# Kernel tuning notes

Measured on AMD Instinct MI355X. Metric: run time of the kernel, lower is better.

Reference implementation:

```python
import jax, jax.numpy as jnp
import numpy as np


def setup_inputs() -> dict:
    key = jax.random.key(0)
    ks = jax.random.split(key, 8)
    B, L, D, H = 4, 2048, 4096, 8
    BW = D // H
    std = 1.0 / np.sqrt(BW)
    x = jax.random.normal(ks[0], (B, L, D), dtype=jnp.float32)
    segment_pos = jax.random.randint(ks[1], (B, L), 0, 1024)
    prev_h = jax.random.normal(ks[2], (B, D), dtype=jnp.float32)
    w_in = jax.random.normal(ks[3], (H, BW, BW), dtype=jnp.float32) * std
    b_in = jnp.zeros((H, BW), dtype=jnp.float32)
    w_a = jax.random.normal(ks[4], (H, BW, BW), dtype=jnp.float32) * std
    b_a = jnp.zeros((H, BW), dtype=jnp.float32)
    # a_param init: uniform on ring [0.9, 0.999], softplus-inverse transform
    unif = jax.random.uniform(ks[5], (D,), dtype=jnp.float32)
    min_rad, max_rad = 0.9, 0.999
    a_real = 0.5 * jnp.log(unif * (max_rad**2 - min_rad**2) + min_rad**2 + 1e-8)
    a_param = jnp.log(jnp.exp(-a_real) - 1.0)
    return {"x": x, "segment_pos": segment_pos, "prev_h": prev_h,
            "w_in": w_in, "b_in": b_in, "w_a": w_a, "b_a": b_a,
            "a_param": a_param}


def _block_diag_linear(x, w, b):
    # x: [B,L,D]; w: [H,BW,BW]; b: [H,BW]
    B, L, D = x.shape
    H = w.shape[0]
    xr = x.reshape(B, L, H, D // H)
    y = jnp.einsum('blhi,hij->blhj', xr, w) + b
    return y.reshape(B, L, D)


def reference(x, segment_pos, prev_h, w_in, b_in, w_a, b_a, a_param):
    # reset indicator at document boundaries (segment_pos == 0)
    reset = (segment_pos == 0).astype(x.dtype)          # [B,L]
    gate_x = jax.nn.sigmoid(_block_diag_linear(x, w_in, b_in))
    gate_a = jax.nn.sigmoid(_block_diag_linear(x, w_a, b_a))
    log_a = -8.0 * gate_a * jax.nn.softplus(a_param)    # [B,L,D]
    a = jnp.exp(log_a)
    multiplier = jnp.sqrt(1.0 - jnp.exp(2.0 * log_a) + 1e-6)
    multiplier = reset[..., None] + (1.0 - reset)[..., None] * multiplier
    normalized_x = x * gate_x * multiplier
    # zero the decay at reset positions (hidden state reset)
    a = a * (1.0 - reset)[..., None]
    # linear recurrence y_t = a_t * y_{t-1} + x_t (initial hidden state = 0,
    # matching the torch L>1 path which does not use prev_h)
    def combine(c1, c2):
        a1, b1 = c1
        a2, b2 = c2
        return (a2 * a1, a2 * b1 + b2)
    _, y = jax.lax.associative_scan(combine, (a, normalized_x), axis=1)
    return y
```

## Files before the change

### kernel.cpp

```cpp
#include <hip/hip_runtime.h>
#include <hip/hip_bf16.h>

typedef _Float16 f16;
typedef _Float16 f16x2 __attribute__((ext_vector_type(2)));
typedef _Float16 f16x4 __attribute__((ext_vector_type(4)));
typedef _Float16 f16x8 __attribute__((ext_vector_type(8)));
typedef float f32x4 __attribute__((ext_vector_type(4)));

#define B_  4
#define L_  2048
#define D_  4096
#define H_  8
#define BW_ 512
#define M_  (B_*L_)
#define CHUNK 128
#define NCH (L_/CHUNK)
#define LOG2E 1.4426950408889634f

static const size_t OFF_WPK   = 0;
static const size_t OFF_MSP   = 8ull<<20;
static const size_t OFF_XH    = 9ull<<20;
static const size_t OFF_YLAP  = 73ull<<20;
static const size_t OFF_SUMA  = 208ull<<20;
static const size_t OFF_SUMY  = 209ull<<20;
static const size_t OFF_CARRY = 210ull<<20;

__device__ __forceinline__ void gl16(const void* g, void* l) {
    __builtin_amdgcn_global_load_lds(
        (const __attribute__((address_space(1))) unsigned int*)g,
        (__attribute__((address_space(3))) unsigned int*)l, 16, 0, 0);
}

__global__ __launch_bounds__(256)
void prep_wpack(const float* __restrict__ w_in, const float* __restrict__ w_a,
                const float* __restrict__ a_param,
                f16* __restrict__ wpk, float* __restrict__ msp2) {
    const int kt  = blockIdx.x & 7;
    const int n32 = (blockIdx.x >> 3) & 15;
    const int h   = blockIdx.x >> 7;
    const int tid = threadIdx.x;
    if (blockIdx.x < 16) {
        int d = blockIdx.x * 256 + tid;
        float v = a_param[d];
        msp2[d] = -8.f * log1pf(expf(v)) * LOG2E;
    }
#pragma unroll
    for (int q = 0; q < 2; ++q) {
        int slot = q * 256 + tid;
        int lane = slot & 63;
        int fidx = slot >> 6;
        int g    = fidx >> 2;
        int fn   = (fidx >> 1) & 1;
        int kk2  = fidx & 1;
        int row = n32 * 32 + fn * 16 + (lane & 15);
        int col = kt * 64 + kk2 * 32 + ((lane >> 4) << 3);
        const float* src = (g ? w_a : w_in) + (size_t)h * BW_ * BW_;
        f16x8 v;
#pragma unroll
        for (int e = 0; e < 8; ++e)
            v[e] = (f16)src[(size_t)(col + e) * BW_ + row];
        size_t o = ((((size_t)(h * 16 + n32) * 8 + kt) * 8) + fidx) * 64 + lane;
        *(f16x8*)(wpk + o * 8) = v;
    }
}

__global__ __launch_bounds__(256)
void prep_xh(const float* __restrict__ x, f16* __restrict__ xh) {
    size_t i = ((size_t)blockIdx.x * 256 + threadIdx.x) * 8;
    size_t stride = (size_t)gridDim.x * 256 * 8;
    for (; i < (size_t)M_ * D_; i += stride) {
        f32x4 v0 = *(const f32x4*)(x + i);
        f32x4 v1 = *(const f32x4*)(x + i + 4);
        f16x8 hv;
        hv[0] = (f16)v0.x; hv[1] = (f16)v0.y; hv[2] = (f16)v0.z; hv[3] = (f16)v0.w;
        hv[4] = (f16)v1.x; hv[5] = (f16)v1.y; hv[6] = (f16)v1.z; hv[7] = (f16)v1.w;
        *(f16x8*)(xh + i) = hv;
    }
}

#define BM 128
#define BN 64
#define BKK 64
#define NT (BW_/BKK)
#define BUFB 16384

#define SMEM_BYTES 36608

__global__ __launch_bounds__(256, 3)
void gemm_gates(const f16*   __restrict__ xh,
                const int*   __restrict__ segpos,
                const f16*   __restrict__ wpk,
                const float* __restrict__ b_in,
                const float* __restrict__ b_a,
                const float* __restrict__ msp2,
                f16x2* __restrict__ ylap,
                float* __restrict__ sumA,
                float* __restrict__ sumY) {
    __shared__ __align__(16) char smem[SMEM_BYTES];
    f16*   om_s = (f16*)smem;
    f16*   xn_s = (f16*)(smem + 16896);
    float* segA = (float*)(smem + 33792);
    float* segY = (float*)(smem + 34944);
    float* rst_s= (float*)(smem + 36096);

    const int tid  = threadIdx.x;
    const int m0   = blockIdx.x * BM;
    const int n0   = blockIdx.y * BN;
    const int h    = blockIdx.z;
    const int lane = tid & 63;
    const int wid  = tid >> 6;
    const int wr   = wid >> 1;
    const int wc   = wid & 1;

    f32x4 accX[4][2] = {};
    f32x4 accA[4][2] = {};

    if (tid < BM) rst_s[tid] = (segpos[m0 + tid] == 0) ? 1.f : 0.f;

    const int grow  = lane >> 3;
    const int gcolS = (((lane & 7) ^ grow) << 3);
    const f16* aSrc = xh + (size_t)(m0 + wid * 32 + grow) * D_ + h * BW_ + gcolS;

    const f16* wbase = wpk + ((size_t)(h * 16) + (n0 >> 5) + wc) * 32768;

    const int swz  = (lane & 7) << 3;
    const int kx   = (lane >> 4) << 3;
    const int arow = wr * 64 + (lane & 15);

    const int rowb = wr * 64 + ((lane >> 4) << 2);
    const int txo = (n0 >> 6) + 1;

    f16x8 bfr[2][8];

    {
        const int k0 = (txo & (NT - 1)) * BKK;
        f16* Asb = (f16*)smem;
#pragma unroll
        for (int q = 0; q < 4; ++q)
            gl16(aSrc + k0 + (size_t)q * 8 * D_, &Asb[(wid * 32 + q * 8) * 64]);
        const f16* tp = wbase + (size_t)(txo & (NT - 1)) * 4096;
#pragma unroll
        for (int j = 0; j < 8; ++j)
            bfr[0][j] = *(const f16x8*)(tp + j * 512 + lane * 8);
    }

#pragma unroll
    for (int t = 0; t < NT; ++t) {
        const int cur = t & 1;
        if (t + 1 < NT) {
            const int kt1 = (t + 1 + txo) & (NT - 1);
            f16* Asb = (f16*)(smem + (cur ^ 1) * BUFB);
#pragma unroll
            for (int q = 0; q < 4; ++q)
                gl16(aSrc + kt1 * BKK + (size_t)q * 8 * D_, &Asb[(wid * 32 + q * 8) * 64]);
            const f16* tp = wbase + (size_t)kt1 * 4096;
#pragma unroll
            for (int j = 0; j < 8; ++j)
                bfr[cur ^ 1][j] = *(const f16x8*)(tp + j * 512 + lane * 8);
            asm volatile("s_waitcnt vmcnt(12)" ::: "memory");
        } else {
            asm volatile("s_waitcnt vmcnt(0)" ::: "memory");
        }
        __builtin_amdgcn_s_barrier();
        __builtin_amdgcn_sched_barrier(0);

        const f16* Asb = (const f16*)(smem + cur * BUFB);
#pragma unroll
        for (int kk2 = 0; kk2 < 2; ++kk2) {
            const int kcolS = (kk2 * 32 + kx) ^ swz;
            f16x8 af[4];
#pragma unroll
            for (int fm = 0; fm < 4; ++fm)
                af[fm] = *(const f16x8*)&Asb[(arow + fm * 16) * 64 + kcolS];
#pragma unroll
            for (int fn = 0; fn < 2; ++fn) {
                f16x8 bx = bfr[cur][fn * 2 + kk2];
                f16x8 ba = bfr[cur][4 + fn * 2 + kk2];
#pragma unroll
                for (int fm = 0; fm < 4; ++fm) {
                    accX[fm][fn] = __builtin_amdgcn_mfma_f32_16x16x32_f16(af[fm], bx, accX[fm][fn], 0, 0, 0);
                    accA[fm][fn] = __builtin_amdgcn_mfma_f32_16x16x32_f16(af[fm], ba, accA[fm][fn], 0, 0, 0);
                }
            }
        }
        __builtin_amdgcn_sched_barrier(0);
        __builtin_amdgcn_s_barrier();
    }

    const f16* As1 = (const f16*)(smem + BUFB);
    f16 xvv[2][4][4];
#pragma unroll
    for (int fn = 0; fn < 2; ++fn) {
        const int ctile = wc * 32 + fn * 16 + (lane & 15);
#pragma unroll
        for (int fm = 0; fm < 4; ++fm)
#pragma unroll
            for (int reg = 0; reg < 4; ++reg) {
                const int rowt = rowb + fm * 16 + reg;
                xvv[fn][fm][reg] = As1[rowt * 64 + (ctile ^ ((rowt & 7) << 3))];
            }
    }
    __syncthreads();

    {
#pragma unroll
        for (int fn = 0; fn < 2; ++fn) {
            const int ctile = wc * 32 + fn * 16 + (lane & 15);
            const int d = h * BW_ + n0 + ctile;
            const float bx = b_in[d];
            const float ba = b_a[d];
            const float mspd = msp2[d];
#pragma unroll
            for (int fm = 0; fm < 4; ++fm) {
#pragma unroll
                for (int reg = 0; reg < 4; ++reg) {
                    const int rowt = rowb + fm * 16 + reg;
                    float gxl = accX[fm][fn][reg] + bx;
                    float gal = accA[fm][fn][reg] + ba;
                    float gx = __builtin_amdgcn_rcpf(1.f + __builtin_amdgcn_exp2f(-gxl * LOG2E));
                    float ga = __builtin_amdgcn_rcpf(1.f + __builtin_amdgcn_exp2f(-gal * LOG2E));
                    float a  = __builtin_amdgcn_exp2f(mspd * ga);
                    float a2 = a * a;
                    float mult = __builtin_amdgcn_sqrtf(1.f + 1e-6f - a2);
                    float rv = rst_s[rowt];
                    a *= (1.f - rv);
                    mult = rv + (1.f - rv) * mult;
                    float xv = (float)xvv[fn][fm][reg];
                    om_s[rowt * 66 + ctile] = (f16)(1.f - a);
                    xn_s[rowt * 66 + ctile] = (f16)(xv * gx * mult);
                }
            }
        }
    }
    __syncthreads();

    const int scol = tid & 63;
    const int sseg = tid >> 6;
    {
        float A = 1.f, yv = 0.f;
#pragma unroll 4
        for (int t = sseg * 32; t < sseg * 32 + 32; ++t) {
            float a  = 1.f - (float)om_s[t * 66 + scol];
            float xn = (float)xn_s[t * 66 + scol];
            yv = fmaf(a, yv, xn);
            A *= a;
        }
        segA[sseg * 72 + scol] = A;
        segY[sseg * 72 + scol] = yv;
    }
    __syncthreads();

    {
        float cy = 0.f, pA = 1.f;
        for (int s = 0; s < sseg; ++s) {
            float As_ = segA[s * 72 + scol];
            float Ys_ = segY[s * 72 + scol];
            cy = fmaf(As_, cy, Ys_);
            pA *= As_;
        }
        float Arun = 1.f, yv = cy;
        const size_t obase = (size_t)(m0 + sseg * 32) * D_ + h * BW_ + n0 + scol;
#pragma unroll 4
        for (int i = 0; i < 32; ++i) {
            const int t = sseg * 32 + i;
            float a  = 1.f - (float)om_s[t * 66 + scol];
            float xn = (float)xn_s[t * 66 + scol];
            yv = fmaf(a, yv, xn);
            Arun *= a;
            f16x2 p;
            p[0] = (f16)yv;
            p[1] = (f16)(pA * Arun);
            ylap[obase + (size_t)i * D_] = p;
        }
        if (sseg == 3) {
            const int bb = m0 >> 11;
            const int cc = (m0 & 2047) >> 7;
            size_t si = ((size_t)bb * NCH + cc) * D_ + h * BW_ + n0 + scol;
            sumA[si] = pA * Arun;
            sumY[si] = yv;
        }
    }
}

__global__ __launch_bounds__(256)
void scan_mid(const float* __restrict__ sumA, const float* __restrict__ sumY,
              float* __restrict__ carry) {
    int d = blockIdx.x * 256 + threadIdx.x;
    int b = blockIdx.y;
    float hcur = 0.f;
#pragma unroll
    for (int c = 0; c < NCH; ++c) {
        size_t si = ((size_t)b * NCH + c) * D_ + d;
        carry[si] = hcur;
        hcur = fmaf(sumA[si], hcur, sumY[si]);
    }
}

__global__ __launch_bounds__(256)
void scan_apply(const float* __restrict__ carry, const f16x2* __restrict__ ylap,
                float* __restrict__ y) {
    size_t i4 = (size_t)blockIdx.x * 256 + threadIdx.x;
    const size_t stride = (size_t)gridDim.x * 256;
    const size_t n4 = (size_t)M_ * D_ / 4;
    for (; i4 < n4; i4 += stride) {
        size_t i = i4 * 4;
        size_t row = i >> 12;
        int d = (int)(i & 4095);
        int b = (int)(row >> 11);
        int c = ((int)row & 2047) >> 7;
        const float* cp = carry + (((size_t)(b * NCH + c)) << 12) + d;
        f32x4 cv = *(const f32x4*)cp;
        f16x8 pk = *(const f16x8*)(ylap + i);
        f32x4 o;
        o.x = fmaf(cv.x, (float)pk[1], (float)pk[0]);
        o.y = fmaf(cv.y, (float)pk[3], (float)pk[2]);
        o.z = fmaf(cv.z, (float)pk[5], (float)pk[4]);
        o.w = fmaf(cv.w, (float)pk[7], (float)pk[6]);
        *(f32x4*)(y + i) = o;
    }
}

extern "C" void kernel_launch(void* const* d_in, const int* in_sizes, int n_in,
                              void* d_out, int out_size, void* d_ws, size_t ws_size,
                              hipStream_t stream) {
    const float* x       = (const float*)d_in[0];
    const int*   segpos  = (const int*)d_in[1];
    const float* w_in    = (const float*)d_in[3];
    const float* b_in    = (const float*)d_in[4];
    const float* w_a     = (const float*)d_in[5];
    const float* b_a     = (const float*)d_in[6];
    const float* a_param = (const float*)d_in[7];

    float* y  = (float*)d_out;
    char*  ws = (char*)d_ws;
    f16*   wpk   = (f16*)(ws + OFF_WPK);
    float* msp2  = (float*)(ws + OFF_MSP);
    f16*   xh    = (f16*)(ws + OFF_XH);
    f16x2* ylap  = (f16x2*)(ws + OFF_YLAP);
    float* sumA  = (float*)(ws + OFF_SUMA);
    float* sumY  = (float*)(ws + OFF_SUMY);
    float* carry = (float*)(ws + OFF_CARRY);

    prep_wpack<<<dim3(1024), 256, 0, stream>>>(w_in, w_a, a_param, wpk, msp2);
    prep_xh<<<dim3(2048), 256, 0, stream>>>(x, xh);
    gemm_gates<<<dim3(M_ / BM, BW_ / BN, H_), 256, 0, stream>>>(
        xh, segpos, wpk, b_in, b_a, msp2, ylap, sumA, sumY);
    scan_mid<<<dim3(D_ / 256, B_), 256, 0, stream>>>(sumA, sumY, carry);
    scan_apply<<<dim3(4096), 256, 0, stream>>>(carry, ylap, y);
}
```

Before: 219.2 us.

## Fuse fp32-to-fp16 conversion of x into GEMM with triple-buffered K pipeline

Drops the separate prep_xh pass that wrote an fp16 copy of x. The gate GEMM now streams fp32 x straight into LDS through global_load_lds, with K tiles cut from 64 to 32 and triple buffering. Values are packed to fp16 in registers before the MFMAs. The grid is reordered so the N-tiles that share an M-tile are adjacent, which should help L2 reuse of x. This removes a full read and write pass over x, at the cost of twice the LDS bytes per K element, more GEMM-side conversion work and round-toward-zero conversion.

```diff
diff --git a/kernel.cpp b/kernel.cpp
--- a/kernel.cpp
+++ b/kernel.cpp
@@ -5,6 +5,7 @@
 typedef _Float16 f16x2 __attribute__((ext_vector_type(2)));
 typedef _Float16 f16x4 __attribute__((ext_vector_type(4)));
 typedef _Float16 f16x8 __attribute__((ext_vector_type(8)));
+typedef __fp16  h16x2 __attribute__((ext_vector_type(2)));
 typedef float f32x4 __attribute__((ext_vector_type(4)));
 
 #define B_  4
@@ -19,11 +20,10 @@
 
 static const size_t OFF_WPK   = 0;
 static const size_t OFF_MSP   = 8ull<<20;
-static const size_t OFF_XH    = 9ull<<20;
-static const size_t OFF_YLAP  = 73ull<<20;
-static const size_t OFF_SUMA  = 208ull<<20;
-static const size_t OFF_SUMY  = 209ull<<20;
-static const size_t OFF_CARRY = 210ull<<20;
+static const size_t OFF_YLAP  = 9ull<<20;
+static const size_t OFF_SUMA  = 144ull<<20;
+static const size_t OFF_SUMY  = 145ull<<20;
+static const size_t OFF_CARRY = 146ull<<20;
 
 __device__ __forceinline__ void gl16(const void* g, void* l) {
     __builtin_amdgcn_global_load_lds(
@@ -64,30 +64,16 @@
     }
 }
 
-__global__ __launch_bounds__(256)
-void prep_xh(const float* __restrict__ x, f16* __restrict__ xh) {
-    size_t i = ((size_t)blockIdx.x * 256 + threadIdx.x) * 8;
-    size_t stride = (size_t)gridDim.x * 256 * 8;
-    for (; i < (size_t)M_ * D_; i += stride) {
-        f32x4 v0 = *(const f32x4*)(x + i);
-        f32x4 v1 = *(const f32x4*)(x + i + 4);
-        f16x8 hv;
-        hv[0] = (f16)v0.x; hv[1] = (f16)v0.y; hv[2] = (f16)v0.z; hv[3] = (f16)v0.w;
-        hv[4] = (f16)v1.x; hv[5] = (f16)v1.y; hv[6] = (f16)v1.z; hv[7] = (f16)v1.w;
-        *(f16x8*)(xh + i) = hv;
-    }
-}
-
 #define BM 128
 #define BN 64
-#define BKK 64
-#define NT (BW_/BKK)
+#define BKK 32
+#define NT 16
 #define BUFB 16384
 
-#define SMEM_BYTES 36608
+#define SMEM_BYTES 49664
 
 __global__ __launch_bounds__(256, 3)
-void gemm_gates(const f16*   __restrict__ xh,
+void gemm_gates(const float* __restrict__ x,
                 const int*   __restrict__ segpos,
                 const f16*   __restrict__ wpk,
                 const float* __restrict__ b_in,
@@ -101,11 +87,11 @@
     f16*   xn_s = (f16*)(smem + 16896);
     float* segA = (float*)(smem + 33792);
     float* segY = (float*)(smem + 34944);
-    float* rst_s= (float*)(smem + 36096);
+    float* rst_s= (float*)(smem + 49152);
 
     const int tid  = threadIdx.x;
-    const int m0   = blockIdx.x * BM;
-    const int n0   = blockIdx.y * BN;
+    const int n0   = blockIdx.x * BN;
+    const int m0   = blockIdx.y * BM;
     const int h    = blockIdx.z;
     const int lane = tid & 63;
     const int wid  = tid >> 6;
@@ -118,86 +104,91 @@
     if (tid < BM) rst_s[tid] = (segpos[m0 + tid] == 0) ? 1.f : 0.f;
 
     const int grow  = lane >> 3;
-    const int gcolS = (((lane & 7) ^ grow) << 3);
-    const f16* aSrc = xh + (size_t)(m0 + wid * 32 + grow) * D_ + h * BW_ + gcolS;
+    const int gcolS = (((lane & 7) ^ grow) << 2);
+    const float* aSrc = x + (size_t)(m0 + wid * 32 + grow) * D_ + h * BW_ + gcolS;
 
     const f16* wbase = wpk + ((size_t)(h * 16) + (n0 >> 5) + wc) * 32768;
 
-    const int swz  = (lane & 7) << 3;
-    const int kx   = (lane >> 4) << 3;
+    const int koff = ((lane >> 4) * 32) ^ ((lane & 7) << 4);
     const int arow = wr * 64 + (lane & 15);
-
     const int rowb = wr * 64 + ((lane >> 4) << 2);
-    const int txo = (n0 >> 6) + 1;
-
-    f16x8 bfr[2][8];
-
-    {
-        const int k0 = (txo & (NT - 1)) * BKK;
-        f16* Asb = (f16*)smem;
-#pragma unroll
-        for (int q = 0; q < 4; ++q)
-            gl16(aSrc + k0 + (size_t)q * 8 * D_, &Asb[(wid * 32 + q * 8) * 64]);
-        const f16* tp = wbase + (size_t)(txo & (NT - 1)) * 4096;
-#pragma unroll
-        for (int j = 0; j < 8; ++j)
-            bfr[0][j] = *(const f16x8*)(tp + j * 512 + lane * 8);
-    }
+    const int txo  = ((n0 >> 5) + 2) & (NT - 1);
+
+    f16x8 bfr[3][4];
+
+#define STAGE(T)                                                              \
+    {                                                                         \
+        const int ktg = ((T) + txo) & (NT - 1);                               \
+        float* Asb = (float*)(smem + ((T) % 3) * BUFB);                       \
+        _Pragma("unroll")                                                     \
+        for (int q = 0; q < 4; ++q)                                           \
+            gl16(aSrc + ktg * 32 + (size_t)q * 8 * D_,                        \
+                 Asb + (wid * 32 + q * 8) * 32);                              \
+        _Pragma("unroll")                                                     \
+        for (int g = 0; g < 2; ++g)                                           \
+            _Pragma("unroll")                                                 \
+            for (int fn = 0; fn < 2; ++fn)                                    \
+                bfr[(T) % 3][g * 2 + fn] = *(const f16x8*)(wbase +            \
+                    ((size_t)(ktg >> 1) * 8 + g * 4 + fn * 2 + (ktg & 1)) *   \
+                        512 + lane * 8);                                      \
+    }
+
+    STAGE(0);
+    STAGE(1);
 
 #pragma unroll
     for (int t = 0; t < NT; ++t) {
-        const int cur = t & 1;
-        if (t + 1 < NT) {
-            const int kt1 = (t + 1 + txo) & (NT - 1);
-            f16* Asb = (f16*)(smem + (cur ^ 1) * BUFB);
-#pragma unroll
-            for (int q = 0; q < 4; ++q)
-                gl16(aSrc + kt1 * BKK + (size_t)q * 8 * D_, &Asb[(wid * 32 + q * 8) * 64]);
-            const f16* tp = wbase + (size_t)kt1 * 4096;
-#pragma unroll
-            for (int j = 0; j < 8; ++j)
-                bfr[cur ^ 1][j] = *(const f16x8*)(tp + j * 512 + lane * 8);
-            asm volatile("s_waitcnt vmcnt(12)" ::: "memory");
-        } else {
-            asm volatile("s_waitcnt vmcnt(0)" ::: "memory");
-        }
+        if (t + 2 < NT) STAGE(t + 2);
+        if (t < NT - 2)      asm volatile("s_waitcnt vmcnt(16)" ::: "memory");
+        else if (t == NT - 2) asm volatile("s_waitcnt vmcnt(8)" ::: "memory");
+        else                  asm volatile("s_waitcnt vmcnt(0)" ::: "memory");
         __builtin_amdgcn_s_barrier();
         __builtin_amdgcn_sched_barrier(0);
 
-        const f16* Asb = (const f16*)(smem + cur * BUFB);
-#pragma unroll
-        for (int kk2 = 0; kk2 < 2; ++kk2) {
-            const int kcolS = (kk2 * 32 + kx) ^ swz;
-            f16x8 af[4];
-#pragma unroll
-            for (int fm = 0; fm < 4; ++fm)
-                af[fm] = *(const f16x8*)&Asb[(arow + fm * 16) * 64 + kcolS];
-#pragma unroll
-            for (int fn = 0; fn < 2; ++fn) {
-                f16x8 bx = bfr[cur][fn * 2 + kk2];
-                f16x8 ba = bfr[cur][4 + fn * 2 + kk2];
-#pragma unroll
-                for (int fm = 0; fm < 4; ++fm) {
-                    accX[fm][fn] = __builtin_amdgcn_mfma_f32_16x16x32_f16(af[fm], bx, accX[fm][fn], 0, 0, 0);
-                    accA[fm][fn] = __builtin_amdgcn_mfma_f32_16x16x32_f16(af[fm], ba, accA[fm][fn], 0, 0, 0);
-                }
+        const char* Asb = smem + (t % 3) * BUFB;
+        f16x8 af[4];
+#pragma unroll
+        for (int fm = 0; fm < 4; ++fm) {
+            const char* rp = Asb + (arow + fm * 16) * 128;
+            f32x4 u0 = *(const f32x4*)(rp + koff);
+            f32x4 u1 = *(const f32x4*)(rp + (koff ^ 16));
+            h16x2 p0 = __builtin_amdgcn_cvt_pkrtz(u0.x, u0.y);
+            h16x2 p1 = __builtin_amdgcn_cvt_pkrtz(u0.z, u0.w);
+            h16x2 p2 = __builtin_amdgcn_cvt_pkrtz(u1.x, u1.y);
+            h16x2 p3 = __builtin_amdgcn_cvt_pkrtz(u1.z, u1.w);
+            f16x8 a8;
+            a8[0] = (f16)p0[0]; a8[1] = (f16)p0[1];
+            a8[2] = (f16)p1[0]; a8[3] = (f16)p1[1];
+            a8[4] = (f16)p2[0]; a8[5] = (f16)p2[1];
+            a8[6] = (f16)p3[0]; a8[7] = (f16)p3[1];
+            af[fm] = a8;
+        }
+#pragma unroll
+        for (int fn = 0; fn < 2; ++fn) {
+            f16x8 bx = bfr[t % 3][fn];
+            f16x8 ba = bfr[t % 3][2 + fn];
+#pragma unroll
+            for (int fm = 0; fm < 4; ++fm) {
+                accX[fm][fn] = __builtin_amdgcn_mfma_f32_16x16x32_f16(af[fm], bx, accX[fm][fn], 0, 0, 0);
+                accA[fm][fn] = __builtin_amdgcn_mfma_f32_16x16x32_f16(af[fm], ba, accA[fm][fn], 0, 0, 0);
             }
         }
         __builtin_amdgcn_sched_barrier(0);
         __builtin_amdgcn_s_barrier();
     }
-
-    const f16* As1 = (const f16*)(smem + BUFB);
-    f16 xvv[2][4][4];
+#undef STAGE
+
+    const float* AsL = (const float*)(smem + (wc ? 0 : 2 * BUFB));
+    float xvv[2][4][4];
 #pragma unroll
     for (int fn = 0; fn < 2; ++fn) {
-        const int ctile = wc * 32 + fn * 16 + (lane & 15);
+        const int c5 = fn * 16 + (lane & 15);
 #pragma unroll
         for (int fm = 0; fm < 4; ++fm)
 #pragma unroll
             for (int reg = 0; reg < 4; ++reg) {
                 const int rowt = rowb + fm * 16 + reg;
-                xvv[fn][fm][reg] = As1[rowt * 64 + (ctile ^ ((rowt & 7) << 3))];
+                xvv[fn][fm][reg] = AsL[rowt * 32 + (c5 ^ ((rowt & 7) << 2))];
             }
     }
     __syncthreads();
@@ -225,7 +216,7 @@
                     float rv = rst_s[rowt];
                     a *= (1.f - rv);
                     mult = rv + (1.f - rv) * mult;
-                    float xv = (float)xvv[fn][fm][reg];
+                    float xv = xvv[fn][fm][reg];
                     om_s[rowt * 66 + ctile] = (f16)(1.f - a);
                     xn_s[rowt * 66 + ctile] = (f16)(xv * gx * mult);
                 }
@@ -335,16 +326,14 @@
     char*  ws = (char*)d_ws;
     f16*   wpk   = (f16*)(ws + OFF_WPK);
     float* msp2  = (float*)(ws + OFF_MSP);
-    f16*   xh    = (f16*)(ws + OFF_XH);
     f16x2* ylap  = (f16x2*)(ws + OFF_YLAP);
     float* sumA  = (float*)(ws + OFF_SUMA);
     float* sumY  = (float*)(ws + OFF_SUMY);
     float* carry = (float*)(ws + OFF_CARRY);
 
     prep_wpack<<<dim3(1024), 256, 0, stream>>>(w_in, w_a, a_param, wpk, msp2);
-    prep_xh<<<dim3(2048), 256, 0, stream>>>(x, xh);
-    gemm_gates<<<dim3(M_ / BM, BW_ / BN, H_), 256, 0, stream>>>(
-        xh, segpos, wpk, b_in, b_a, msp2, ylap, sumA, sumY);
+    gemm_gates<<<dim3(BW_ / BN, M_ / BM, H_), 256, 0, stream>>>(
+        x, segpos, wpk, b_in, b_a, msp2, ylap, sumA, sumY);
     scan_mid<<<dim3(D_ / 256, B_), 256, 0, stream>>>(sumA, sumY, carry);
     scan_apply<<<dim3(4096), 256, 0, stream>>>(carry, ylap, y);
 }
```

Result: slower. 242.5 us (+10.6%).

## Triple-buffer A tiles in gate GEMM and merge prep kernels into one launch

Applied to the files above, without the earlier changes.

The gate GEMM moves from double to triple buffering of the x tiles in LDS, issuing loads two k-steps ahead and retuning the vmcnt waits. The epilogue now reads the final tile from buffer 0, and the start offset txo changes so the last tile maps to the column block the epilogue needs. The weight-pack and x-to-fp16 prep kernels are fused into one launch to save a kernel boundary. LDS per block grows to about 49.6KB, which may lower occupancy below the 3 blocks per CU the launch bounds target.

```diff
diff --git a/kernel.cpp b/kernel.cpp
--- a/kernel.cpp
+++ b/kernel.cpp
@@ -32,49 +32,50 @@
 }
 
 __global__ __launch_bounds__(256)
-void prep_wpack(const float* __restrict__ w_in, const float* __restrict__ w_a,
-                const float* __restrict__ a_param,
-                f16* __restrict__ wpk, float* __restrict__ msp2) {
-    const int kt  = blockIdx.x & 7;
-    const int n32 = (blockIdx.x >> 3) & 15;
-    const int h   = blockIdx.x >> 7;
+void prep_all(const float* __restrict__ w_in, const float* __restrict__ w_a,
+              const float* __restrict__ a_param, const float* __restrict__ x,
+              f16* __restrict__ wpk, float* __restrict__ msp2,
+              f16* __restrict__ xh) {
+    const int bid = blockIdx.x;
     const int tid = threadIdx.x;
-    if (blockIdx.x < 16) {
-        int d = blockIdx.x * 256 + tid;
-        float v = a_param[d];
-        msp2[d] = -8.f * log1pf(expf(v)) * LOG2E;
-    }
-#pragma unroll
-    for (int q = 0; q < 2; ++q) {
-        int slot = q * 256 + tid;
-        int lane = slot & 63;
-        int fidx = slot >> 6;
-        int g    = fidx >> 2;
-        int fn   = (fidx >> 1) & 1;
-        int kk2  = fidx & 1;
-        int row = n32 * 32 + fn * 16 + (lane & 15);
-        int col = kt * 64 + kk2 * 32 + ((lane >> 4) << 3);
-        const float* src = (g ? w_a : w_in) + (size_t)h * BW_ * BW_;
-        f16x8 v;
-#pragma unroll
-        for (int e = 0; e < 8; ++e)
-            v[e] = (f16)src[(size_t)(col + e) * BW_ + row];
-        size_t o = ((((size_t)(h * 16 + n32) * 8 + kt) * 8) + fidx) * 64 + lane;
-        *(f16x8*)(wpk + o * 8) = v;
-    }
-}
-
-__global__ __launch_bounds__(256)
-void prep_xh(const float* __restrict__ x, f16* __restrict__ xh) {
-    size_t i = ((size_t)blockIdx.x * 256 + threadIdx.x) * 8;
-    size_t stride = (size_t)gridDim.x * 256 * 8;
-    for (; i < (size_t)M_ * D_; i += stride) {
-        f32x4 v0 = *(const f32x4*)(x + i);
-        f32x4 v1 = *(const f32x4*)(x + i + 4);
-        f16x8 hv;
-        hv[0] = (f16)v0.x; hv[1] = (f16)v0.y; hv[2] = (f16)v0.z; hv[3] = (f16)v0.w;
-        hv[4] = (f16)v1.x; hv[5] = (f16)v1.y; hv[6] = (f16)v1.z; hv[7] = (f16)v1.w;
-        *(f16x8*)(xh + i) = hv;
+    if (bid < 1024) {
+        const int kt  = bid & 7;
+        const int n32 = (bid >> 3) & 15;
+        const int h   = bid >> 7;
+        if (bid < 16) {
+            int d = bid * 256 + tid;
+            float v = a_param[d];
+            msp2[d] = -8.f * log1pf(expf(v)) * LOG2E;
+        }
+#pragma unroll
+        for (int q = 0; q < 2; ++q) {
+            int slot = q * 256 + tid;
+            int lane = slot & 63;
+            int fidx = slot >> 6;
+            int g    = fidx >> 2;
+            int fn   = (fidx >> 1) & 1;
+            int kk2  = fidx & 1;
+            int row = n32 * 32 + fn * 16 + (lane & 15);
+            int col = kt * 64 + kk2 * 32 + ((lane >> 4) << 3);
+            const float* src = (g ? w_a : w_in) + (size_t)h * BW_ * BW_;
+            f16x8 v;
+#pragma unroll
+            for (int e = 0; e < 8; ++e)
+                v[e] = (f16)src[(size_t)(col + e) * BW_ + row];
+            size_t o = ((((size_t)(h * 16 + n32) * 8 + kt) * 8) + fidx) * 64 + lane;
+            *(f16x8*)(wpk + o * 8) = v;
+        }
+    } else {
+        size_t i = ((size_t)(bid - 1024) * 256 + tid) * 8;
+        const size_t stride = (size_t)2048 * 256 * 8;
+        for (; i < (size_t)M_ * D_; i += stride) {
+            f32x4 v0 = *(const f32x4*)(x + i);
+            f32x4 v1 = *(const f32x4*)(x + i + 4);
+            f16x8 hv;
+            hv[0] = (f16)v0.x; hv[1] = (f16)v0.y; hv[2] = (f16)v0.z; hv[3] = (f16)v0.w;
+            hv[4] = (f16)v1.x; hv[5] = (f16)v1.y; hv[6] = (f16)v1.z; hv[7] = (f16)v1.w;
+            *(f16x8*)(xh + i) = hv;
+        }
     }
 }
 
@@ -84,7 +85,7 @@
 #define NT (BW_/BKK)
 #define BUFB 16384
 
-#define SMEM_BYTES 36608
+#define SMEM_BYTES 49664
 
 __global__ __launch_bounds__(256, 3)
 void gemm_gates(const f16*   __restrict__ xh,
@@ -101,7 +102,7 @@
     f16*   xn_s = (f16*)(smem + 16896);
     float* segA = (float*)(smem + 33792);
     float* segY = (float*)(smem + 34944);
-    float* rst_s= (float*)(smem + 36096);
+    float* rst_s= (float*)(smem + 49152);
 
     const int tid  = threadIdx.x;
     const int m0   = blockIdx.x * BM;
@@ -126,45 +127,44 @@
     const int swz  = (lane & 7) << 3;
     const int kx   = (lane >> 4) << 3;
     const int arow = wr * 64 + (lane & 15);
-
     const int rowb = wr * 64 + ((lane >> 4) << 2);
-    const int txo = (n0 >> 6) + 1;
+    const int txo  = (n0 >> 6) + 2;
 
     f16x8 bfr[2][8];
 
-    {
-        const int k0 = (txo & (NT - 1)) * BKK;
-        f16* Asb = (f16*)smem;
-#pragma unroll
-        for (int q = 0; q < 4; ++q)
-            gl16(aSrc + k0 + (size_t)q * 8 * D_, &Asb[(wid * 32 + q * 8) * 64]);
-        const f16* tp = wbase + (size_t)(txo & (NT - 1)) * 4096;
-#pragma unroll
-        for (int j = 0; j < 8; ++j)
-            bfr[0][j] = *(const f16x8*)(tp + j * 512 + lane * 8);
-    }
+#define STAGE_A(T)                                                            \
+    {                                                                         \
+        const int ktg = ((T) + txo) & (NT - 1);                               \
+        f16* Asb = (f16*)(smem + ((T) % 3) * BUFB);                           \
+        _Pragma("unroll")                                                     \
+        for (int q = 0; q < 4; ++q)                                           \
+            gl16(aSrc + ktg * BKK + (size_t)q * 8 * D_,                       \
+                 &Asb[(wid * 32 + q * 8) * 64]);                              \
+    }
+#define LOAD_B(T)                                                             \
+    {                                                                         \
+        const int ktg = ((T) + txo) & (NT - 1);                               \
+        const f16* tp = wbase + (size_t)ktg * 4096;                           \
+        _Pragma("unroll")                                                     \
+        for (int j = 0; j < 8; ++j)                                           \
+            bfr[(T) & 1][j] = *(const f16x8*)(tp + j * 512 + lane * 8);       \
+    }
+
+    STAGE_A(0);
+    LOAD_B(0);
+    STAGE_A(1);
 
 #pragma unroll
     for (int t = 0; t < NT; ++t) {
-        const int cur = t & 1;
-        if (t + 1 < NT) {
-            const int kt1 = (t + 1 + txo) & (NT - 1);
-            f16* Asb = (f16*)(smem + (cur ^ 1) * BUFB);
-#pragma unroll
-            for (int q = 0; q < 4; ++q)
-                gl16(aSrc + kt1 * BKK + (size_t)q * 8 * D_, &Asb[(wid * 32 + q * 8) * 64]);
-            const f16* tp = wbase + (size_t)kt1 * 4096;
-#pragma unroll
-            for (int j = 0; j < 8; ++j)
-                bfr[cur ^ 1][j] = *(const f16x8*)(tp + j * 512 + lane * 8);
-            asm volatile("s_waitcnt vmcnt(12)" ::: "memory");
-        } else {
-            asm volatile("s_waitcnt vmcnt(0)" ::: "memory");
-        }
+        if (t + 1 < NT) LOAD_B(t + 1);
+        if (t + 2 < NT) STAGE_A(t + 2);
+        if (t < NT - 2)       asm volatile("s_waitcnt vmcnt(16)" ::: "memory");
+        else if (t == NT - 2) asm volatile("s_waitcnt vmcnt(12)" ::: "memory");
+        else                  asm volatile("s_waitcnt vmcnt(0)"  ::: "memory");
         __builtin_amdgcn_s_barrier();
         __builtin_amdgcn_sched_barrier(0);
 
-        const f16* Asb = (const f16*)(smem + cur * BUFB);
+        const f16* Asb = (const f16*)(smem + (t % 3) * BUFB);
 #pragma unroll
         for (int kk2 = 0; kk2 < 2; ++kk2) {
             const int kcolS = (kk2 * 32 + kx) ^ swz;
@@ -174,8 +174,8 @@
                 af[fm] = *(const f16x8*)&Asb[(arow + fm * 16) * 64 + kcolS];
 #pragma unroll
             for (int fn = 0; fn < 2; ++fn) {
-                f16x8 bx = bfr[cur][fn * 2 + kk2];
-                f16x8 ba = bfr[cur][4 + fn * 2 + kk2];
+                f16x8 bx = bfr[t & 1][fn * 2 + kk2];
+                f16x8 ba = bfr[t & 1][4 + fn * 2 + kk2];
 #pragma unroll
                 for (int fm = 0; fm < 4; ++fm) {
                     accX[fm][fn] = __builtin_amdgcn_mfma_f32_16x16x32_f16(af[fm], bx, accX[fm][fn], 0, 0, 0);
@@ -186,8 +186,10 @@
         __builtin_amdgcn_sched_barrier(0);
         __builtin_amdgcn_s_barrier();
     }
-
-    const f16* As1 = (const f16*)(smem + BUFB);
+#undef STAGE_A
+#undef LOAD_B
+
+    const f16* As1 = (const f16*)smem;
     f16 xvv[2][4][4];
 #pragma unroll
     for (int fn = 0; fn < 2; ++fn) {
@@ -341,8 +343,7 @@
     float* sumY  = (float*)(ws + OFF_SUMY);
     float* carry = (float*)(ws + OFF_CARRY);
 
-    prep_wpack<<<dim3(1024), 256, 0, stream>>>(w_in, w_a, a_param, wpk, msp2);
-    prep_xh<<<dim3(2048), 256, 0, stream>>>(x, xh);
+    prep_all<<<dim3(3072), 256, 0, stream>>>(w_in, w_a, a_param, x, wpk, msp2, xh);
     gemm_gates<<<dim3(M_ / BM, BW_ / BN, H_), 256, 0, stream>>>(
         xh, segpos, wpk, b_in, b_a, msp2, ylap, sumA, sumY);
     scan_mid<<<dim3(D_ / 256, B_), 256, 0, stream>>>(sumA, sumY, carry);
```

Result: faster. 213.6 us (-2.6%).
